# Kernel optimization log

Measured on AMD Instinct MI355X. Metric: run time of the kernel, lower is better.

Reference implementation:

```python
import jax, jax.numpy as jnp
import numpy as np

# PQMatcher forward (cleaned): per passage timestep i, additive (Bahdanau-style)
# attention over all question positions:
#   x = tanh(Wp(Up[i]) + Wq(Uq) + Wv(v));  s = x . v;  a = softmax(s over lq)
#   c[i] = a @ Uq
# The original python loop over i is loop-invariant except Wp(Up[i]), so it
# vectorizes exactly into one broadcasted tanh + einsum. (The original also
# computed a duplicate s_/a_ from Upr==Up and Uqr==Uq which is identical math
# and unused; we compute it once.)

LP, LQ, BZ, SZ, H = 400, 50, 32, 768, 128


def setup_inputs() -> dict:
    key = jax.random.key(0)
    ks = jax.random.split(key, 9)
    s_in = 1.0 / np.sqrt(SZ)
    s_h = 1.0 / np.sqrt(H)
    return {
        "Up": jax.random.normal(ks[0], (LP, BZ, SZ), jnp.float32),
        "Uq": jax.random.normal(ks[1], (LQ, BZ, SZ), jnp.float32),
        "Wp_w": jax.random.normal(ks[2], (H, SZ), jnp.float32) * s_in,
        "Wp_b": jax.random.normal(ks[3], (H,), jnp.float32) * s_in,
        "Wq_w": jax.random.normal(ks[4], (H, SZ), jnp.float32) * s_in,
        "Wq_b": jax.random.normal(ks[5], (H,), jnp.float32) * s_in,
        "Wv_w": jax.random.normal(ks[6], (H, H), jnp.float32) * s_h,
        "Wv_b": jax.random.normal(ks[7], (H,), jnp.float32) * s_h,
        "v": jax.random.normal(ks[8], (BZ, H), jnp.float32),
    }


def reference(Up, Uq, Wp_w, Wp_b, Wq_w, Wq_b, Wv_w, Wv_b, v):
    # Projections (loop-invariant parts hoisted out of the original loop)
    Wup = jnp.einsum("pbs,hs->pbh", Up, Wp_w) + Wp_b  # [lp, bz, h]
    Wuq = jnp.einsum("qbs,hs->qbh", Uq, Wq_w) + Wq_b  # [lq, bz, h]
    Wvv = jnp.einsum("bh,gh->bg", v, Wv_w) + Wv_b      # [bz, h]
    # tanh score fusion: [lp, lq, bz, h]
    x = jnp.tanh(Wup[:, None, :, :] + Wuq[None, :, :, :] + Wvv[None, None, :, :])
    # scores s[i] = x[i] . v  -> [lp, bz, lq]
    s = jnp.einsum("pqbh,bh->pbq", x, v)
    a = jax.nn.softmax(s, axis=-1)                      # softmax over question len
    # contexts c[i] = a[i] @ Uq -> [lp, bz, sz]
    c = jnp.einsum("pbq,qbs->pbs", a, Uq)
    return c
```

## Files before the change

### kernel.cpp

```cpp
#include <hip/hip_runtime.h>

#define LP 400
#define LQ 50
#define BZ 32
#define SZ 768
#define HH 128
#define PROWS 14464

typedef unsigned short u16;
typedef __attribute__((ext_vector_type(8))) short short8;
typedef __attribute__((ext_vector_type(4))) float f32x4;

__device__ __forceinline__ float fexp2(float x) {
#if __has_builtin(__builtin_amdgcn_exp2f)
  return __builtin_amdgcn_exp2f(x);
#else
  return exp2f(x);
#endif
}
__device__ __forceinline__ float frcp(float x) {
#if __has_builtin(__builtin_amdgcn_rcpf)
  return __builtin_amdgcn_rcpf(x);
#else
  return 1.0f / x;
#endif
}

__device__ __forceinline__ unsigned pack2(float x, float y) {
  return (__float_as_uint(x) >> 16) | (__float_as_uint(y) & 0xffff0000u);
}
__device__ __forceinline__ float remf(float x) {
  return x - __uint_as_float(__float_as_uint(x) & 0xffff0000u);
}

__global__ __launch_bounds__(256) void prep_kernel(
    const float* __restrict__ Wp_w, const float* __restrict__ Wq_w,
    const float* __restrict__ v, const float* __restrict__ Wv_w,
    const float* __restrict__ Wv_b,
    u16* __restrict__ Wph, u16* __restrict__ Wpl,
    u16* __restrict__ Wqh, u16* __restrict__ Wql, float* __restrict__ Wvv) {
  const int bx = blockIdx.x, t = threadIdx.x;
  if (bx < 96) {
    int gid = bx * 256 + t;
    int base = gid * 8;
    const float* src;
    u16 *dh, *dl;
    if (base < HH * SZ) {
      src = Wp_w + base; dh = Wph + base; dl = Wpl + base;
    } else {
      int o = base - HH * SZ;
      src = Wq_w + o; dh = Wqh + o; dl = Wql + o;
    }
    float4 x0 = *(const float4*)src;
    float4 x1 = *(const float4*)(src + 4);
    uint4 H, L;
    H.x = pack2(x0.x, x0.y); H.y = pack2(x0.z, x0.w);
    H.z = pack2(x1.x, x1.y); H.w = pack2(x1.z, x1.w);
    L.x = pack2(remf(x0.x), remf(x0.y)); L.y = pack2(remf(x0.z), remf(x0.w));
    L.z = pack2(remf(x1.x), remf(x1.y)); L.w = pack2(remf(x1.z), remf(x1.w));
    *(uint4*)dh = H;
    *(uint4*)dl = L;
  } else {
    int id = (bx - 96) * 256 + t;
    int b = id >> 7, g = id & 127;
    const float4* vb = reinterpret_cast<const float4*>(v + b * HH);
    const float4* wr = reinterpret_cast<const float4*>(Wv_w + g * HH);
    float s = Wv_b[g];
#pragma unroll
    for (int i = 0; i < HH / 4; ++i) {
      float4 a = vb[i], w = wr[i];
      s = fmaf(a.x, w.x, s); s = fmaf(a.y, w.y, s);
      s = fmaf(a.z, w.z, s); s = fmaf(a.w, w.w, s);
    }
    Wvv[id] = s;
  }
}

__global__ __launch_bounds__(256, 1) void mfma_gemm(
    const float* __restrict__ Up, const float* __restrict__ Uq,
    const u16* __restrict__ Wph, const u16* __restrict__ Wpl,
    const u16* __restrict__ Wqh, const u16* __restrict__ Wql,
    float* __restrict__ partial) {
  __shared__ u16 Ah[128][40], Al[128][40], Bh[128][40], Bl[128][40];
  const int t = threadIdx.x, lane = t & 63, wid = t >> 6;
  const int bx = blockIdx.x, z = blockIdx.y;
  const int m0 = bx * 128;
  const bool probq = (bx >= 100);
  const u16* WH = probq ? Wqh : Wph;
  const u16* WL = probq ? Wql : Wpl;
  const int k0base = z * 384;

  const int ra = t >> 1, kh = (t & 1) * 16;
  const int grow = m0 + ra;
  const float* srcA = nullptr;
  if (grow < 12800) srcA = Up + grow * SZ;
  else if (grow < 14400) srcA = Uq + (grow - 12800) * SZ;
  const u16* srcWH = WH + ra * SZ;
  const u16* srcWL = WL + ra * SZ;

  const int wm = (wid >> 1) * 64, wn = (wid & 1) * 64;
  const int fr = lane & 15, fg = lane >> 4;

  f32x4 acc[4][4];
#pragma unroll
  for (int i = 0; i < 4; ++i)
#pragma unroll
    for (int j = 0; j < 4; ++j) acc[i][j] = (f32x4){0.f, 0.f, 0.f, 0.f};

  float4 a0, a1, a2, a3;
  uint4 wh0, wh1, wl0, wl1;

#define GLOAD(s)                                                         \
  do {                                                                   \
    int kk = k0base + (s) * 32 + kh;                                     \
    if (srcA) {                                                          \
      a0 = *(const float4*)(srcA + kk);                                  \
      a1 = *(const float4*)(srcA + kk + 4);                              \
      a2 = *(const float4*)(srcA + kk + 8);                              \
      a3 = *(const float4*)(srcA + kk + 12);                             \
    } else {                                                             \
      a0 = a1 = a2 = a3 = make_float4(0.f, 0.f, 0.f, 0.f);               \
    }                                                                    \
    wh0 = *(const uint4*)(srcWH + kk); wh1 = *(const uint4*)(srcWH + kk + 8); \
    wl0 = *(const uint4*)(srcWL + kk); wl1 = *(const uint4*)(srcWL + kk + 8); \
  } while (0)

#define WSTORE()                                                          \
  do {                                                                    \
    uint4 H0, H1, L0, L1;                                                 \
    H0.x = pack2(a0.x, a0.y); H0.y = pack2(a0.z, a0.w);                   \
    H0.z = pack2(a1.x, a1.y); H0.w = pack2(a1.z, a1.w);                   \
    H1.x = pack2(a2.x, a2.y); H1.y = pack2(a2.z, a2.w);                   \
    H1.z = pack2(a3.x, a3.y); H1.w = pack2(a3.z, a3.w);                   \
    L0.x = pack2(remf(a0.x), remf(a0.y)); L0.y = pack2(remf(a0.z), remf(a0.w)); \
    L0.z = pack2(remf(a1.x), remf(a1.y)); L0.w = pack2(remf(a1.z), remf(a1.w)); \
    L1.x = pack2(remf(a2.x), remf(a2.y)); L1.y = pack2(remf(a2.z), remf(a2.w)); \
    L1.z = pack2(remf(a3.x), remf(a3.y)); L1.w = pack2(remf(a3.z), remf(a3.w)); \
    *(uint4*)&Ah[ra][kh] = H0; *(uint4*)&Ah[ra][kh + 8] = H1;             \
    *(uint4*)&Al[ra][kh] = L0; *(uint4*)&Al[ra][kh + 8] = L1;             \
    *(uint4*)&Bh[ra][kh] = wh0; *(uint4*)&Bh[ra][kh + 8] = wh1;           \
    *(uint4*)&Bl[ra][kh] = wl0; *(uint4*)&Bl[ra][kh + 8] = wl1;           \
  } while (0)

  GLOAD(0);
  WSTORE();
  __syncthreads();

  for (int s = 0; s < 12; ++s) {
    if (s < 11) GLOAD(s + 1);
    short8 ah[4], al[4], bh[4], bl[4];
#pragma unroll
    for (int i = 0; i < 4; ++i) {
      ah[i] = *(const short8*)&Ah[wm + i * 16 + fr][fg * 8];
      al[i] = *(const short8*)&Al[wm + i * 16 + fr][fg * 8];
      bh[i] = *(const short8*)&Bh[wn + i * 16 + fr][fg * 8];
      bl[i] = *(const short8*)&Bl[wn + i * 16 + fr][fg * 8];
    }
#pragma unroll
    for (int i = 0; i < 4; ++i)
#pragma unroll
      for (int j = 0; j < 4; ++j) {
        acc[i][j] = __builtin_amdgcn_mfma_f32_16x16x32_bf16(ah[i], bh[j], acc[i][j], 0, 0, 0);
        acc[i][j] = __builtin_amdgcn_mfma_f32_16x16x32_bf16(ah[i], bl[j], acc[i][j], 0, 0, 0);
        acc[i][j] = __builtin_amdgcn_mfma_f32_16x16x32_bf16(al[i], bh[j], acc[i][j], 0, 0, 0);
      }
    __syncthreads();
    if (s < 11) WSTORE();
    __syncthreads();
  }
#undef GLOAD
#undef WSTORE

  float* pz = partial + (size_t)z * (PROWS * HH);
#pragma unroll
  for (int i = 0; i < 4; ++i) {
    int r0 = m0 + wm + i * 16 + fg * 4;
#pragma unroll
    for (int j = 0; j < 4; ++j) {
      int c = wn + j * 16 + fr;
#pragma unroll
      for (int e = 0; e < 4; ++e) pz[(r0 + e) * HH + c] = acc[i][j][e];
    }
  }
}

__global__ __launch_bounds__(256) void w2prep_kernel(
    const float* __restrict__ partial, const float* __restrict__ Wq_b,
    const float* __restrict__ Wvv, float* __restrict__ W2B, float TS) {
  int idx = blockIdx.x * 256 + threadIdx.x;
  int rr = idx >> 5, h = (idx & 31) * 4;
  int row = 12800 + rr, b = rr & 31;
  float4 p0 = *(const float4*)&partial[(size_t)row * HH + h];
  float4 p1 = *(const float4*)&partial[(size_t)(PROWS + row) * HH + h];
  float4 bb = *(const float4*)&Wq_b[h];
  float4 wv = *(const float4*)&Wvv[b * HH + h];
  float4 r;
  r.x = (p0.x + p1.x + bb.x + wv.x) * TS;
  r.y = (p0.y + p1.y + bb.y + wv.y) * TS;
  r.z = (p0.z + p1.z + bb.z + wv.z) * TS;
  r.w = (p0.w + p1.w + bb.w + wv.w) * TS;
  *(float4*)&W2B[(size_t)rr * HH + h] = r;
}

__global__ __launch_bounds__(256) void score_ctx(
    const float* __restrict__ partial, const float* __restrict__ Wp_b,
    const float* __restrict__ W2B, const float* __restrict__ v,
    const float* __restrict__ Uq, float* __restrict__ out, float TS) {
  const int f = blockIdx.x;
  const int b = (f & 7) * 4 + ((f >> 3) & 3);
  const int pbase = (f >> 5) * 16;
  const int t = threadIdx.x, lane = t & 63, w = t >> 6;
  __shared__ float W2s[LQ][129];
  __shared__ float Wps[16][HH];
  __shared__ float vsh[HH];
  __shared__ float as[16][52];

  for (int ff = t; ff < LQ * 32; ff += 256) {
    int q = ff >> 5, c4 = ff & 31;
    float4 x = *(const float4*)&W2B[(size_t)(q * BZ + b) * HH + c4 * 4];
    W2s[q][c4 * 4 + 0] = x.x; W2s[q][c4 * 4 + 1] = x.y;
    W2s[q][c4 * 4 + 2] = x.z; W2s[q][c4 * 4 + 3] = x.w;
  }
  for (int ff = t; ff < 16 * 32; ff += 256) {
    int i = ff >> 5, c4 = ff & 31;
    int grow = (pbase + i) * BZ + b;
    float4 p0 = *(const float4*)&partial[(size_t)grow * HH + c4 * 4];
    float4 p1 = *(const float4*)&partial[(size_t)(PROWS + grow) * HH + c4 * 4];
    float4 bb = *(const float4*)&Wp_b[c4 * 4];
    float4 r;
    r.x = (p0.x + p1.x + bb.x) * TS; r.y = (p0.y + p1.y + bb.y) * TS;
    r.z = (p0.z + p1.z + bb.z) * TS; r.w = (p0.w + p1.w + bb.w) * TS;
    *(float4*)&Wps[i][c4 * 4] = r;
  }
  if (t < 32) *(float4*)&vsh[t * 4] = *(const float4*)&v[b * HH + t * 4];
  __syncthreads();

  const int q = (lane < LQ) ? lane : (LQ - 1);
  const int prow = w * 4;
  float A0 = 0.f, A1 = 0.f, A2 = 0.f, A3 = 0.f;
  for (int h = 0; h < HH; h += 4) {
#pragma unroll
    for (int j = 0; j < 4; ++j) {
      float w2 = W2s[q][h + j];
      float vj = vsh[h + j];
      float r0 = frcp(fexp2(Wps[prow + 0][h + j] + w2) + 1.f);
      float r1 = frcp(fexp2(Wps[prow + 1][h + j] + w2) + 1.f);
      float r2 = frcp(fexp2(Wps[prow + 2][h + j] + w2) + 1.f);
      float r3 = frcp(fexp2(Wps[prow + 3][h + j] + w2) + 1.f);
      A0 = fmaf(vj, r0, A0); A1 = fmaf(vj, r1, A1);
      A2 = fmaf(vj, r2, A2); A3 = fmaf(vj, r3, A3);
    }
  }

#define SOFTMAX(AR, PI)                                                   \
  do {                                                                    \
    float a = (lane < LQ) ? (AR) : 1e30f;                                 \
    float mn = a;                                                         \
    mn = fminf(mn, __shfl_xor(mn, 1));  mn = fminf(mn, __shfl_xor(mn, 2)); \
    mn = fminf(mn, __shfl_xor(mn, 4));  mn = fminf(mn, __shfl_xor(mn, 8)); \
    mn = fminf(mn, __shfl_xor(mn, 16)); mn = fminf(mn, __shfl_xor(mn, 32)); \
    float e = fexp2((mn - a) * TS);         \
    float sm = e;                                                         \
    sm += __shfl_xor(sm, 1);  sm += __shfl_xor(sm, 2);                    \
    sm += __shfl_xor(sm, 4);  sm += __shfl_xor(sm, 8);                    \
    sm += __shfl_xor(sm, 16); sm += __shfl_xor(sm, 32);                   \
    float val = e * frcp(sm);                                             \
    if (lane < LQ) as[prow + (PI)][lane] = val;                           \
  } while (0)

  SOFTMAX(A0, 0); SOFTMAX(A1, 1); SOFTMAX(A2, 2); SOFTMAX(A3, 3);
#undef SOFTMAX
  __syncthreads();

  if (t < 192) {
    const int s4 = t * 4;
    f32x4 acc[16];
#pragma unroll
    for (int i = 0; i < 16; ++i) acc[i] = (f32x4){0.f, 0.f, 0.f, 0.f};
    for (int qp = 0; qp < LQ; qp += 2) {
      float4 u0 = *(const float4*)&Uq[(size_t)(qp * BZ + b) * SZ + s4];
      float4 u1 = *(const float4*)&Uq[(size_t)((qp + 1) * BZ + b) * SZ + s4];
#pragma unroll
      for (int i = 0; i < 16; ++i) {
        float2 a2 = *(const float2*)&as[i][qp];
        acc[i][0] = fmaf(a2.x, u0.x, acc[i][0]); acc[i][1] = fmaf(a2.x, u0.y, acc[i][1]);
        acc[i][2] = fmaf(a2.x, u0.z, acc[i][2]); acc[i][3] = fmaf(a2.x, u0.w, acc[i][3]);
        acc[i][0] = fmaf(a2.y, u1.x, acc[i][0]); acc[i][1] = fmaf(a2.y, u1.y, acc[i][1]);
        acc[i][2] = fmaf(a2.y, u1.z, acc[i][2]); acc[i][3] = fmaf(a2.y, u1.w, acc[i][3]);
      }
    }
#pragma unroll
    for (int i = 0; i < 16; ++i) {
      float4 r = make_float4(acc[i][0], acc[i][1], acc[i][2], acc[i][3]);
      *(float4*)&out[(size_t)((pbase + i) * BZ + b) * SZ + s4] = r;
    }
  }
}

extern "C" void kernel_launch(void* const* d_in, const int* in_sizes, int n_in,
                              void* d_out, int out_size, void* d_ws, size_t ws_size,
                              hipStream_t stream) {
  const float* Up   = (const float*)d_in[0];
  const float* Uq   = (const float*)d_in[1];
  const float* Wp_w = (const float*)d_in[2];
  const float* Wp_b = (const float*)d_in[3];
  const float* Wq_w = (const float*)d_in[4];
  const float* Wq_b = (const float*)d_in[5];
  const float* Wv_w = (const float*)d_in[6];
  const float* Wv_b = (const float*)d_in[7];
  const float* v    = (const float*)d_in[8];
  float* out = (float*)d_out;

  float* ws      = (float*)d_ws;
  float* Wvv     = ws;
  float* W2B     = Wvv + BZ * HH;
  u16* Wph       = (u16*)(W2B + LQ * BZ * HH);
  u16* Wpl       = Wph + HH * SZ;
  u16* Wqh       = Wpl + HH * SZ;
  u16* Wql       = Wqh + HH * SZ;
  float* partial = (float*)(Wql + HH * SZ);

  const float TS = 2.8853900817779268f;

  prep_kernel<<<dim3(112), dim3(256), 0, stream>>>(
      Wp_w, Wq_w, v, Wv_w, Wv_b, Wph, Wpl, Wqh, Wql, Wvv);
  mfma_gemm<<<dim3(113, 2), dim3(256), 0, stream>>>(
      Up, Uq, Wph, Wpl, Wqh, Wql, partial);
  w2prep_kernel<<<dim3(200), dim3(256), 0, stream>>>(partial, Wq_b, Wvv, W2B, TS);
  score_ctx<<<dim3(800), dim3(256), 0, stream>>>(
      partial, Wp_b, W2B, v, Uq, out, TS);
}
```

Measured before the change: 175.4 us.

## Shrink GEMM tiles, fuse W2 prep into score kernel, halve passage rows per block

Result: no change. 174.3 us (-0.7%).

```diff
diff --git a/kernel.cpp b/kernel.cpp
--- a/kernel.cpp
+++ b/kernel.cpp
@@ -5,7 +5,7 @@
 #define BZ 32
 #define SZ 768
 #define HH 128
-#define PROWS 14464
+#define PR_TOT 14400
 
 typedef unsigned short u16;
 typedef __attribute__((ext_vector_type(8))) short short8;
@@ -76,34 +76,34 @@
   }
 }
 
-__global__ __launch_bounds__(256, 1) void mfma_gemm(
+__global__ __launch_bounds__(256, 2) void mfma_gemm(
     const float* __restrict__ Up, const float* __restrict__ Uq,
     const u16* __restrict__ Wph, const u16* __restrict__ Wpl,
     const u16* __restrict__ Wqh, const u16* __restrict__ Wql,
     float* __restrict__ partial) {
-  __shared__ u16 Ah[128][40], Al[128][40], Bh[128][40], Bl[128][40];
+  __shared__ u16 Ah[64][40], Al[64][40], Bh[128][40], Bl[128][40];
   const int t = threadIdx.x, lane = t & 63, wid = t >> 6;
   const int bx = blockIdx.x, z = blockIdx.y;
-  const int m0 = bx * 128;
-  const bool probq = (bx >= 100);
+  const int m0 = bx * 64;
+  const bool probq = (bx >= 200);
   const u16* WH = probq ? Wqh : Wph;
   const u16* WL = probq ? Wql : Wpl;
   const int k0base = z * 384;
 
   const int ra = t >> 1, kh = (t & 1) * 16;
-  const int grow = m0 + ra;
-  const float* srcA = nullptr;
-  if (grow < 12800) srcA = Up + grow * SZ;
-  else if (grow < 14400) srcA = Uq + (grow - 12800) * SZ;
+  const bool hasA = (ra < 64);
+  const int grow = m0 + (ra & 63);
+  const float* srcA = (grow < 12800) ? (Up + (size_t)grow * SZ)
+                                     : (Uq + (size_t)(grow - 12800) * SZ);
   const u16* srcWH = WH + ra * SZ;
   const u16* srcWL = WL + ra * SZ;
 
-  const int wm = (wid >> 1) * 64, wn = (wid & 1) * 64;
+  const int wm = (wid >> 1) * 32, wn = (wid & 1) * 64;
   const int fr = lane & 15, fg = lane >> 4;
 
-  f32x4 acc[4][4];
-#pragma unroll
-  for (int i = 0; i < 4; ++i)
+  f32x4 acc[2][4];
+#pragma unroll
+  for (int i = 0; i < 2; ++i)
 #pragma unroll
     for (int j = 0; j < 4; ++j) acc[i][j] = (f32x4){0.f, 0.f, 0.f, 0.f};
 
@@ -113,13 +113,11 @@
 #define GLOAD(s)                                                         \
   do {                                                                   \
     int kk = k0base + (s) * 32 + kh;                                     \
-    if (srcA) {                                                          \
+    if (hasA) {                                                          \
       a0 = *(const float4*)(srcA + kk);                                  \
       a1 = *(const float4*)(srcA + kk + 4);                              \
       a2 = *(const float4*)(srcA + kk + 8);                              \
       a3 = *(const float4*)(srcA + kk + 12);                             \
-    } else {                                                             \
-      a0 = a1 = a2 = a3 = make_float4(0.f, 0.f, 0.f, 0.f);               \
     }                                                                    \
     wh0 = *(const uint4*)(srcWH + kk); wh1 = *(const uint4*)(srcWH + kk + 8); \
     wl0 = *(const uint4*)(srcWL + kk); wl1 = *(const uint4*)(srcWL + kk + 8); \
@@ -127,17 +125,19 @@
 
 #define WSTORE()                                                          \
   do {                                                                    \
-    uint4 H0, H1, L0, L1;                                                 \
-    H0.x = pack2(a0.x, a0.y); H0.y = pack2(a0.z, a0.w);                   \
-    H0.z = pack2(a1.x, a1.y); H0.w = pack2(a1.z, a1.w);                   \
-    H1.x = pack2(a2.x, a2.y); H1.y = pack2(a2.z, a2.w);                   \
-    H1.z = pack2(a3.x, a3.y); H1.w = pack2(a3.z, a3.w);                   \
-    L0.x = pack2(remf(a0.x), remf(a0.y)); L0.y = pack2(remf(a0.z), remf(a0.w)); \
-    L0.z = pack2(remf(a1.x), remf(a1.y)); L0.w = pack2(remf(a1.z), remf(a1.w)); \
-    L1.x = pack2(remf(a2.x), remf(a2.y)); L1.y = pack2(remf(a2.z), remf(a2.w)); \
-    L1.z = pack2(remf(a3.x), remf(a3.y)); L1.w = pack2(remf(a3.z), remf(a3.w)); \
-    *(uint4*)&Ah[ra][kh] = H0; *(uint4*)&Ah[ra][kh + 8] = H1;             \
-    *(uint4*)&Al[ra][kh] = L0; *(uint4*)&Al[ra][kh + 8] = L1;             \
+    if (hasA) {                                                           \
+      uint4 H0, H1, L0, L1;                                               \
+      H0.x = pack2(a0.x, a0.y); H0.y = pack2(a0.z, a0.w);                 \
+      H0.z = pack2(a1.x, a1.y); H0.w = pack2(a1.z, a1.w);                 \
+      H1.x = pack2(a2.x, a2.y); H1.y = pack2(a2.z, a2.w);                 \
+      H1.z = pack2(a3.x, a3.y); H1.w = pack2(a3.z, a3.w);                 \
+      L0.x = pack2(remf(a0.x), remf(a0.y)); L0.y = pack2(remf(a0.z), remf(a0.w)); \
+      L0.z = pack2(remf(a1.x), remf(a1.y)); L0.w = pack2(remf(a1.z), remf(a1.w)); \
+      L1.x = pack2(remf(a2.x), remf(a2.y)); L1.y = pack2(remf(a2.z), remf(a2.w)); \
+      L1.z = pack2(remf(a3.x), remf(a3.y)); L1.w = pack2(remf(a3.z), remf(a3.w)); \
+      *(uint4*)&Ah[ra][kh] = H0; *(uint4*)&Ah[ra][kh + 8] = H1;           \
+      *(uint4*)&Al[ra][kh] = L0; *(uint4*)&Al[ra][kh + 8] = L1;           \
+    }                                                                     \
     *(uint4*)&Bh[ra][kh] = wh0; *(uint4*)&Bh[ra][kh + 8] = wh1;           \
     *(uint4*)&Bl[ra][kh] = wl0; *(uint4*)&Bl[ra][kh + 8] = wl1;           \
   } while (0)
@@ -148,16 +148,19 @@
 
   for (int s = 0; s < 12; ++s) {
     if (s < 11) GLOAD(s + 1);
-    short8 ah[4], al[4], bh[4], bl[4];
-#pragma unroll
-    for (int i = 0; i < 4; ++i) {
+    short8 ah[2], al[2], bh[4], bl[4];
+#pragma unroll
+    for (int i = 0; i < 2; ++i) {
       ah[i] = *(const short8*)&Ah[wm + i * 16 + fr][fg * 8];
       al[i] = *(const short8*)&Al[wm + i * 16 + fr][fg * 8];
-      bh[i] = *(const short8*)&Bh[wn + i * 16 + fr][fg * 8];
-      bl[i] = *(const short8*)&Bl[wn + i * 16 + fr][fg * 8];
-    }
-#pragma unroll
-    for (int i = 0; i < 4; ++i)
+    }
+#pragma unroll
+    for (int j = 0; j < 4; ++j) {
+      bh[j] = *(const short8*)&Bh[wn + j * 16 + fr][fg * 8];
+      bl[j] = *(const short8*)&Bl[wn + j * 16 + fr][fg * 8];
+    }
+#pragma unroll
+    for (int i = 0; i < 2; ++i)
 #pragma unroll
       for (int j = 0; j < 4; ++j) {
         acc[i][j] = __builtin_amdgcn_mfma_f32_16x16x32_bf16(ah[i], bh[j], acc[i][j], 0, 0, 0);
@@ -171,85 +174,79 @@
 #undef GLOAD
 #undef WSTORE
 
-  float* pz = partial + (size_t)z * (PROWS * HH);
-#pragma unroll
-  for (int i = 0; i < 4; ++i) {
+  float* pz = partial + (size_t)z * (PR_TOT * HH);
+#pragma unroll
+  for (int i = 0; i < 2; ++i) {
     int r0 = m0 + wm + i * 16 + fg * 4;
 #pragma unroll
     for (int j = 0; j < 4; ++j) {
       int c = wn + j * 16 + fr;
 #pragma unroll
-      for (int e = 0; e < 4; ++e) pz[(r0 + e) * HH + c] = acc[i][j][e];
-    }
-  }
-}
-
-__global__ __launch_bounds__(256) void w2prep_kernel(
-    const float* __restrict__ partial, const float* __restrict__ Wq_b,
-    const float* __restrict__ Wvv, float* __restrict__ W2B, float TS) {
-  int idx = blockIdx.x * 256 + threadIdx.x;
-  int rr = idx >> 5, h = (idx & 31) * 4;
-  int row = 12800 + rr, b = rr & 31;
-  float4 p0 = *(const float4*)&partial[(size_t)row * HH + h];
-  float4 p1 = *(const float4*)&partial[(size_t)(PROWS + row) * HH + h];
-  float4 bb = *(const float4*)&Wq_b[h];
-  float4 wv = *(const float4*)&Wvv[b * HH + h];
-  float4 r;
-  r.x = (p0.x + p1.x + bb.x + wv.x) * TS;
-  r.y = (p0.y + p1.y + bb.y + wv.y) * TS;
-  r.z = (p0.z + p1.z + bb.z + wv.z) * TS;
-  r.w = (p0.w + p1.w + bb.w + wv.w) * TS;
-  *(float4*)&W2B[(size_t)rr * HH + h] = r;
-}
-
-__global__ __launch_bounds__(256) void score_ctx(
+      for (int e = 0; e < 4; ++e) pz[(size_t)(r0 + e) * HH + c] = acc[i][j][e];
+    }
+  }
+}
+
+__global__ __launch_bounds__(256, 4) void score_ctx(
     const float* __restrict__ partial, const float* __restrict__ Wp_b,
-    const float* __restrict__ W2B, const float* __restrict__ v,
-    const float* __restrict__ Uq, float* __restrict__ out, float TS) {
+    const float* __restrict__ Wq_b, const float* __restrict__ Wvv,
+    const float* __restrict__ v, const float* __restrict__ Uq,
+    float* __restrict__ out, float TS) {
   const int f = blockIdx.x;
-  const int b = (f & 7) * 4 + ((f >> 3) & 3);
-  const int pbase = (f >> 5) * 16;
+  const int b = ((f & 7) << 2) | ((f >> 3) & 3);
+  const int pbase = (f >> 5) * 8;
   const int t = threadIdx.x, lane = t & 63, w = t >> 6;
-  __shared__ float W2s[LQ][129];
-  __shared__ float Wps[16][HH];
-  __shared__ float vsh[HH];
-  __shared__ float as[16][52];
+  __shared__ float W2s[HH][52];
+  __shared__ f32x4 Wps4[8][32];
+  __shared__ f32x4 vsh4[32];
+  __shared__ float as_[8][52];
 
   for (int ff = t; ff < LQ * 32; ff += 256) {
-    int q = ff >> 5, c4 = ff & 31;
-    float4 x = *(const float4*)&W2B[(size_t)(q * BZ + b) * HH + c4 * 4];
-    W2s[q][c4 * 4 + 0] = x.x; W2s[q][c4 * 4 + 1] = x.y;
-    W2s[q][c4 * 4 + 2] = x.z; W2s[q][c4 * 4 + 3] = x.w;
-  }
-  for (int ff = t; ff < 16 * 32; ff += 256) {
-    int i = ff >> 5, c4 = ff & 31;
-    int grow = (pbase + i) * BZ + b;
-    float4 p0 = *(const float4*)&partial[(size_t)grow * HH + c4 * 4];
-    float4 p1 = *(const float4*)&partial[(size_t)(PROWS + grow) * HH + c4 * 4];
+    int q_ = ff % LQ, c4 = ff / LQ;
+    size_t row = 12800 + (size_t)(q_ * BZ + b);
+    float4 p0 = *(const float4*)&partial[row * HH + c4 * 4];
+    float4 p1 = *(const float4*)&partial[((size_t)PR_TOT + row) * HH + c4 * 4];
+    float4 bb = *(const float4*)&Wq_b[c4 * 4];
+    float4 wv = *(const float4*)&Wvv[b * HH + c4 * 4];
+    W2s[c4 * 4 + 0][q_] = (p0.x + p1.x + bb.x + wv.x) * TS;
+    W2s[c4 * 4 + 1][q_] = (p0.y + p1.y + bb.y + wv.y) * TS;
+    W2s[c4 * 4 + 2][q_] = (p0.z + p1.z + bb.z + wv.z) * TS;
+    W2s[c4 * 4 + 3][q_] = (p0.w + p1.w + bb.w + wv.w) * TS;
+  }
+  {
+    int i = t >> 5, c4 = t & 31;
+    size_t grow = (size_t)(pbase + i) * BZ + b;
+    float4 p0 = *(const float4*)&partial[grow * HH + c4 * 4];
+    float4 p1 = *(const float4*)&partial[((size_t)PR_TOT + grow) * HH + c4 * 4];
     float4 bb = *(const float4*)&Wp_b[c4 * 4];
-    float4 r;
-    r.x = (p0.x + p1.x + bb.x) * TS; r.y = (p0.y + p1.y + bb.y) * TS;
-    r.z = (p0.z + p1.z + bb.z) * TS; r.w = (p0.w + p1.w + bb.w) * TS;
-    *(float4*)&Wps[i][c4 * 4] = r;
-  }
-  if (t < 32) *(float4*)&vsh[t * 4] = *(const float4*)&v[b * HH + t * 4];
+    Wps4[i][c4] = (f32x4){(p0.x + p1.x + bb.x) * TS, (p0.y + p1.y + bb.y) * TS,
+                          (p0.z + p1.z + bb.z) * TS, (p0.w + p1.w + bb.w) * TS};
+  }
+  if (t < 32) {
+    float4 x = *(const float4*)&v[b * HH + t * 4];
+    vsh4[t] = (f32x4){x.x, x.y, x.z, x.w};
+  }
   __syncthreads();
 
   const int q = (lane < LQ) ? lane : (LQ - 1);
-  const int prow = w * 4;
-  float A0 = 0.f, A1 = 0.f, A2 = 0.f, A3 = 0.f;
-  for (int h = 0; h < HH; h += 4) {
-#pragma unroll
-    for (int j = 0; j < 4; ++j) {
-      float w2 = W2s[q][h + j];
-      float vj = vsh[h + j];
-      float r0 = frcp(fexp2(Wps[prow + 0][h + j] + w2) + 1.f);
-      float r1 = frcp(fexp2(Wps[prow + 1][h + j] + w2) + 1.f);
-      float r2 = frcp(fexp2(Wps[prow + 2][h + j] + w2) + 1.f);
-      float r3 = frcp(fexp2(Wps[prow + 3][h + j] + w2) + 1.f);
-      A0 = fmaf(vj, r0, A0); A1 = fmaf(vj, r1, A1);
-      A2 = fmaf(vj, r2, A2); A3 = fmaf(vj, r3, A3);
-    }
+  const int prow = w * 2;
+  float A0 = 0.f, A1 = 0.f;
+  for (int h4 = 0; h4 < 32; ++h4) {
+    f32x4 vj = vsh4[h4];
+    f32x4 w0 = Wps4[prow][h4];
+    f32x4 w1 = Wps4[prow + 1][h4];
+    float s0 = W2s[h4 * 4 + 0][q];
+    float s1 = W2s[h4 * 4 + 1][q];
+    float s2 = W2s[h4 * 4 + 2][q];
+    float s3 = W2s[h4 * 4 + 3][q];
+    A0 = fmaf(vj[0], frcp(fexp2(w0[0] + s0) + 1.f), A0);
+    A0 = fmaf(vj[1], frcp(fexp2(w0[1] + s1) + 1.f), A0);
+    A0 = fmaf(vj[2], frcp(fexp2(w0[2] + s2) + 1.f), A0);
+    A0 = fmaf(vj[3], frcp(fexp2(w0[3] + s3) + 1.f), A0);
+    A1 = fmaf(vj[0], frcp(fexp2(w1[0] + s0) + 1.f), A1);
+    A1 = fmaf(vj[1], frcp(fexp2(w1[1] + s1) + 1.f), A1);
+    A1 = fmaf(vj[2], frcp(fexp2(w1[2] + s2) + 1.f), A1);
+    A1 = fmaf(vj[3], frcp(fexp2(w1[3] + s3) + 1.f), A1);
   }
 
 #define SOFTMAX(AR, PI)                                                   \
@@ -265,24 +262,24 @@
     sm += __shfl_xor(sm, 4);  sm += __shfl_xor(sm, 8);                    \
     sm += __shfl_xor(sm, 16); sm += __shfl_xor(sm, 32);                   \
     float val = e * frcp(sm);                                             \
-    if (lane < LQ) as[prow + (PI)][lane] = val;                           \
+    if (lane < LQ) as_[prow + (PI)][lane] = val;                          \
   } while (0)
 
-  SOFTMAX(A0, 0); SOFTMAX(A1, 1); SOFTMAX(A2, 2); SOFTMAX(A3, 3);
+  SOFTMAX(A0, 0); SOFTMAX(A1, 1);
 #undef SOFTMAX
   __syncthreads();
 
   if (t < 192) {
     const int s4 = t * 4;
-    f32x4 acc[16];
-#pragma unroll
-    for (int i = 0; i < 16; ++i) acc[i] = (f32x4){0.f, 0.f, 0.f, 0.f};
+    f32x4 acc[8];
+#pragma unroll
+    for (int i = 0; i < 8; ++i) acc[i] = (f32x4){0.f, 0.f, 0.f, 0.f};
     for (int qp = 0; qp < LQ; qp += 2) {
       float4 u0 = *(const float4*)&Uq[(size_t)(qp * BZ + b) * SZ + s4];
       float4 u1 = *(const float4*)&Uq[(size_t)((qp + 1) * BZ + b) * SZ + s4];
 #pragma unroll
-      for (int i = 0; i < 16; ++i) {
-        float2 a2 = *(const float2*)&as[i][qp];
+      for (int i = 0; i < 8; ++i) {
+        float2 a2 = *(const float2*)&as_[i][qp];
         acc[i][0] = fmaf(a2.x, u0.x, acc[i][0]); acc[i][1] = fmaf(a2.x, u0.y, acc[i][1]);
         acc[i][2] = fmaf(a2.x, u0.z, acc[i][2]); acc[i][3] = fmaf(a2.x, u0.w, acc[i][3]);
         acc[i][0] = fmaf(a2.y, u1.x, acc[i][0]); acc[i][1] = fmaf(a2.y, u1.y, acc[i][1]);
@@ -290,7 +287,7 @@
       }
     }
 #pragma unroll
-    for (int i = 0; i < 16; ++i) {
+    for (int i = 0; i < 8; ++i) {
       float4 r = make_float4(acc[i][0], acc[i][1], acc[i][2], acc[i][3]);
       *(float4*)&out[(size_t)((pbase + i) * BZ + b) * SZ + s4] = r;
     }
@@ -313,8 +310,7 @@
 
   float* ws      = (float*)d_ws;
   float* Wvv     = ws;
-  float* W2B     = Wvv + BZ * HH;
-  u16* Wph       = (u16*)(W2B + LQ * BZ * HH);
+  u16* Wph       = (u16*)(Wvv + BZ * HH);
   u16* Wpl       = Wph + HH * SZ;
   u16* Wqh       = Wpl + HH * SZ;
   u16* Wql       = Wqh + HH * SZ;
@@ -324,9 +320,8 @@
 
   prep_kernel<<<dim3(112), dim3(256), 0, stream>>>(
       Wp_w, Wq_w, v, Wv_w, Wv_b, Wph, Wpl, Wqh, Wql, Wvv);
-  mfma_gemm<<<dim3(113, 2), dim3(256), 0, stream>>>(
+  mfma_gemm<<<dim3(225, 2), dim3(256), 0, stream>>>(
       Up, Uq, Wph, Wpl, Wqh, Wql, partial);
-  w2prep_kernel<<<dim3(200), dim3(256), 0, stream>>>(partial, Wq_b, Wvv, W2B, TS);
-  score_ctx<<<dim3(800), dim3(256), 0, stream>>>(
-      partial, Wp_b, W2B, v, Uq, out, TS);
-}
+  score_ctx<<<dim3(1600), dim3(256), 0, stream>>>(
+      partial, Wp_b, Wq_b, Wvv, v, Uq, out, TS);
+}
```
